# Kernel tuning notes

Measured on AMD Instinct MI355X. Metric: run time of the kernel, lower is better.

The kernel has to match this reference:

```python
import jax, jax.numpy as jnp
import numpy as np

N_EMBD = 1024
HEAD_SIZE = 64

def setup_inputs() -> dict:
    key = jax.random.key(0)
    kx, kk, kq, kv = jax.random.split(key, 4)
    B, T = 8, 2048
    x = jax.random.normal(kx, (B, T, N_EMBD), dtype=jnp.float32)
    s = 1.0 / np.sqrt(N_EMBD)  # torch Linear default init scale (kaiming-uniform-ish)
    Wk = jax.random.uniform(kk, (N_EMBD, HEAD_SIZE), jnp.float32, -s, s)
    Wq = jax.random.uniform(kq, (N_EMBD, HEAD_SIZE), jnp.float32, -s, s)
    Wv = jax.random.uniform(kv, (N_EMBD, HEAD_SIZE), jnp.float32, -s, s)
    return {"x": x, "Wk": Wk, "Wq": Wq, "Wv": Wv}

def reference(x, Wk, Wq, Wv):
    # x: (B,T,C); projections to (B,T,H)
    k = jnp.einsum('btc,ch->bth', x, Wk)
    q = jnp.einsum('btc,ch->bth', x, Wq)
    v = jnp.einsum('btc,ch->bth', x, Wv)
    T = x.shape[1]
    scale = k.shape[-1] ** -0.5
    wei = jnp.einsum('bth,bsh->bts', q, k) * scale  # (B,T,T)
    causal = jnp.tril(jnp.ones((T, T), dtype=bool))
    wei = jnp.where(causal, wei, -jnp.inf)
    wei = jax.nn.softmax(wei, axis=-1)
    out = jnp.einsum('bts,bsh->bth', wei, v)  # (B,T,H)
    return out
```

## Files before the change

kernel.cpp:

```cpp
#include <hip/hip_runtime.h>
#include <math.h>

namespace {
constexpr int BATCH = 8;
constexpr int TSEQ  = 2048;
constexpr int CDIM  = 1024;
constexpr int HDIM  = 64;
constexpr int MROWS = BATCH * TSEQ;
constexpr int NTILE = 128;
constexpr int NSLC  = 4;
constexpr float QSCALE = 0.125f * 1.4426950408889634f;
}

typedef __attribute__((ext_vector_type(4))) float  f32x4;
typedef __attribute__((ext_vector_type(8))) short  s16x8;
typedef __attribute__((ext_vector_type(4))) unsigned short u16x4;

__device__ __forceinline__ unsigned short f2bf(float f) {
    union { float f; unsigned u; } c{f};
    unsigned r = c.u + 0x7FFFu + ((c.u >> 16) & 1u);
    return (unsigned short)(r >> 16);
}

__global__ __launch_bounds__(256)
void wswz_kernel(const float* __restrict__ Wk, const float* __restrict__ Wq,
                 const float* __restrict__ Wv, unsigned short* __restrict__ swz)
{
    const int idx  = blockIdx.x * 256 + threadIdx.x;
    const int j    = idx & 7;
    const int lane = (idx >> 3) & 63;
    const int rest = idx >> 9;
    const int tn   = rest % 12;
    const int ksg  = rest / 12;
    const int kk   = ksg * 32 + (lane >> 4) * 8 + j;
    const int n    = tn * 16 + (lane & 15);
    float val;
    if (n < 64)       val = Wq[kk * HDIM + n] * QSCALE;
    else if (n < 128) val = Wk[kk * HDIM + (n - 64)];
    else              val = Wv[kk * HDIM + (n - 128)];
    swz[idx] = f2bf(val);
}

__global__ __launch_bounds__(512, 4)
void proj_kernel(const float* __restrict__ x, const unsigned short* __restrict__ swz,
                 unsigned short* __restrict__ q, unsigned short* __restrict__ k,
                 unsigned short* __restrict__ vt)
{
    __shared__ unsigned short xl[32][1032];

    const int tid  = threadIdx.x;
    const int lane = tid & 63, wave = tid >> 6;
    const int quad = lane >> 4, l15 = lane & 15;
    const int mh   = wave >> 2;
    const int cq   = wave & 3;
    const int m0   = blockIdx.x * 32;

    {
        const float* xb = x + (size_t)m0 * CDIM;
        float4 t[16];
        #pragma unroll
        for (int i = 0; i < 16; ++i)
            t[i] = *(const float4*)(xb + i * 2048 + tid * 4);
        #pragma unroll
        for (int i = 0; i < 16; ++i) {
            const int o = i * 2048 + tid * 4;
            u16x4 p;
            p[0] = f2bf(t[i].x); p[1] = f2bf(t[i].y);
            p[2] = f2bf(t[i].z); p[3] = f2bf(t[i].w);
            *(u16x4*)&xl[o >> 10][o & 1023] = p;
        }
    }
    __syncthreads();

    f32x4 acc[3] = {};
    const unsigned short* bp = swz + ((size_t)(cq * 3) * 64 + lane) * 8;
    s16x8 b0 = *(const s16x8*)(bp);
    s16x8 b1 = *(const s16x8*)(bp + 512);
    s16x8 b2 = *(const s16x8*)(bp + 1024);
    bp += 6144;

    #pragma unroll
    for (int ks = 0; ks < 32; ++ks) {
        s16x8 nb0, nb1, nb2;
        if (ks < 31) {
            nb0 = *(const s16x8*)(bp);
            nb1 = *(const s16x8*)(bp + 512);
            nb2 = *(const s16x8*)(bp + 1024);
            bp += 6144;
        }
        const s16x8 af = *(const s16x8*)&xl[mh * 16 + l15][ks * 32 + quad * 8];
        acc[0] = __builtin_amdgcn_mfma_f32_16x16x32_bf16(af, b0, acc[0], 0, 0, 0);
        acc[1] = __builtin_amdgcn_mfma_f32_16x16x32_bf16(af, b1, acc[1], 0, 0, 0);
        acc[2] = __builtin_amdgcn_mfma_f32_16x16x32_bf16(af, b2, acc[2], 0, 0, 0);
        if (ks < 31) { b0 = nb0; b1 = nb1; b2 = nb2; }
    }

    const int rowg = m0 + mh * 16 + quad * 4;
    #pragma unroll
    for (int t = 0; t < 3; ++t) {
        const int n = cq * 48 + t * 16 + l15;
        if (n < 64) {
            #pragma unroll
            for (int r = 0; r < 4; ++r)
                q[(size_t)(rowg + r) * HDIM + n] = f2bf(acc[t][r]);
        } else if (n < 128) {
            #pragma unroll
            for (int r = 0; r < 4; ++r)
                k[(size_t)(rowg + r) * HDIM + (n - 64)] = f2bf(acc[t][r]);
        } else {
            const int h  = n - 128;
            const int bb = rowg >> 11, tl = rowg & 2047;
            u16x4 pv;
            #pragma unroll
            for (int r = 0; r < 4; ++r) pv[r] = f2bf(acc[t][r]);
            *(u16x4*)(vt + ((size_t)bb * HDIM + h) * TSEQ + tl) = pv;
        }
    }
}

__global__ __launch_bounds__(256, 2)
void attn_part(const unsigned short* __restrict__ q, const unsigned short* __restrict__ k,
               const unsigned short* __restrict__ vt, float* __restrict__ Opart,
               float* __restrict__ lpart)
{
    __shared__ unsigned short Kb[2][4096];
    __shared__ unsigned short Vb[2][4096];
    __shared__ unsigned short Pl[4][16][72];

    const int tid  = threadIdx.x;
    const int lane = tid & 63, wave = tid >> 6;
    const int quad = lane >> 4, l15 = lane & 15;
    const int b    = blockIdx.y;
    const int p    = blockIdx.x >> 2;
    const int s    = blockIdx.x & 3;

    const unsigned short* qb  = q  + (size_t)b * TSEQ * HDIM;
    const unsigned short* kb  = k  + (size_t)b * TSEQ * HDIM;
    const unsigned short* vtb = vt + (size_t)b * HDIM * TSEQ;

    const int rs = tid >> 3, cgs = tid & 7;
    const int d0 = (((cgs >> 2) * 4 + (rs >> 4)) * 64 + (cgs & 3) * 16 + (rs & 15)) * 8;
    const int rs2 = rs + 32;
    const int d1 = (((cgs >> 2) * 4 + (rs2 >> 4)) * 64 + (cgs & 3) * 16 + (rs2 & 15)) * 8;

    for (int tsel = 0; tsel < 2; ++tsel) {
        const int t   = (tsel == 0) ? p : 31 - p;
        const int m0w = t * 64 + wave * 16;
        const int nt  = t + 1;

        s16x8 aq0 = *(const s16x8*)(qb + (size_t)(m0w + l15) * HDIM + quad * 8);
        s16x8 aq1 = *(const s16x8*)(qb + (size_t)(m0w + l15) * HDIM + 32 + quad * 8);

        f32x4 O[4] = {};
        float l_lane[4] = {0.f, 0.f, 0.f, 0.f};

        if (s < nt) {
            {
                const int n0 = s * 64;
                const s16x8 ka = *(const s16x8*)(kb + (size_t)(n0 + rs) * HDIM + cgs * 8);
                const s16x8 kc = *(const s16x8*)(kb + (size_t)(n0 + rs2) * HDIM + cgs * 8);
                const s16x8 va = *(const s16x8*)(vtb + (size_t)rs * TSEQ + n0 + cgs * 8);
                const s16x8 vc = *(const s16x8*)(vtb + (size_t)rs2 * TSEQ + n0 + cgs * 8);
                *(s16x8*)&Kb[0][d0] = ka; *(s16x8*)&Kb[0][d1] = kc;
                *(s16x8*)&Vb[0][d0] = va; *(s16x8*)&Vb[0][d1] = vc;
            }
            __syncthreads();

            int cur = 0;
            for (int c = s; c < nt; c += 4) {
                const int cn = c + 4;
                const bool pref = cn < nt;
                s16x8 ka, kc, va, vc;
                if (pref) {
                    const int n0n = cn * 64;
                    ka = *(const s16x8*)(kb + (size_t)(n0n + rs) * HDIM + cgs * 8);
                    kc = *(const s16x8*)(kb + (size_t)(n0n + rs2) * HDIM + cgs * 8);
                    va = *(const s16x8*)(vtb + (size_t)rs * TSEQ + n0n + cgs * 8);
                    vc = *(const s16x8*)(vtb + (size_t)rs2 * TSEQ + n0n + cgs * 8);
                }

                const unsigned short* Kc = Kb[cur];
                const unsigned short* Vc = Vb[cur];
                f32x4 S[4] = {};
                #pragma unroll
                for (int st = 0; st < 4; ++st) {
                    const s16x8 k0 = *(const s16x8*)&Kc[(st * 64 + lane) * 8];
                    const s16x8 k1 = *(const s16x8*)&Kc[((4 + st) * 64 + lane) * 8];
                    S[st] = __builtin_amdgcn_mfma_f32_16x16x32_bf16(aq0, k0, S[st], 0, 0, 0);
                    S[st] = __builtin_amdgcn_mfma_f32_16x16x32_bf16(aq1, k1, S[st], 0, 0, 0);
                }

                const int n0 = c * 64;
                if (c == t) {
                    const int rowbase = m0w + quad * 4;
                    #pragma unroll
                    for (int st = 0; st < 4; ++st) {
                        const int col = n0 + st * 16 + l15;
                        #pragma unroll
                        for (int r = 0; r < 4; ++r) {
                            const float pv = (col > rowbase + r) ? 0.f : exp2f(S[st][r]);
                            S[st][r] = pv;
                            l_lane[r] += pv;
                        }
                    }
                } else {
                    #pragma unroll
                    for (int st = 0; st < 4; ++st)
                        #pragma unroll
                        for (int r = 0; r < 4; ++r) {
                            const float pv = exp2f(S[st][r]);
                            S[st][r] = pv;
                            l_lane[r] += pv;
                        }
                }

                #pragma unroll
                for (int st = 0; st < 4; ++st)
                    #pragma unroll
                    for (int r = 0; r < 4; ++r)
                        Pl[wave][quad * 4 + r][st * 16 + l15] = f2bf(S[st][r]);
                const s16x8 pa0 = *(const s16x8*)&Pl[wave][l15][quad * 8];
                const s16x8 pa1 = *(const s16x8*)&Pl[wave][l15][32 + quad * 8];

                #pragma unroll
                for (int hst = 0; hst < 4; ++hst) {
                    const s16x8 v0 = *(const s16x8*)&Vc[(hst * 64 + lane) * 8];
                    const s16x8 v1 = *(const s16x8*)&Vc[((4 + hst) * 64 + lane) * 8];
                    O[hst] = __builtin_amdgcn_mfma_f32_16x16x32_bf16(pa0, v0, O[hst], 0, 0, 0);
                    O[hst] = __builtin_amdgcn_mfma_f32_16x16x32_bf16(pa1, v1, O[hst], 0, 0, 0);
                }

                if (pref) {
                    *(s16x8*)&Kb[1 - cur][d0] = ka; *(s16x8*)&Kb[1 - cur][d1] = kc;
                    *(s16x8*)&Vb[1 - cur][d0] = va; *(s16x8*)&Vb[1 - cur][d1] = vc;
                }
                __syncthreads();
                cur ^= 1;
            }
        }

        #pragma unroll
        for (int off = 1; off < 16; off <<= 1)
            #pragma unroll
            for (int r = 0; r < 4; ++r)
                l_lane[r] += __shfl_xor(l_lane[r], off);

        const int ti16 = t * 4 + wave;
        const size_t pi = ((size_t)b * NTILE + ti16) * NSLC + s;
        #pragma unroll
        for (int hst = 0; hst < 4; ++hst)
            #pragma unroll
            for (int r = 0; r < 4; ++r)
                Opart[(pi * 16 + quad * 4 + r) * HDIM + hst * 16 + l15] = O[hst][r];
        if (l15 == 0) {
            #pragma unroll
            for (int r = 0; r < 4; ++r)
                lpart[pi * 16 + quad * 4 + r] = l_lane[r];
        }
    }
}

__global__ __launch_bounds__(256)
void attn_combine(const float* __restrict__ Opart, const float* __restrict__ lpart,
                  float* __restrict__ out)
{
    const int g   = blockIdx.x * 256 + threadIdx.x;
    const int row = g >> 4;
    const int c4  = (g & 15) << 2;
    const int b   = row >> 11, t = row & 2047;
    const int ti  = t >> 4,  r = t & 15;
    const size_t p0 = ((size_t)b * NTILE + ti) * NSLC;

    float4 acc = {0.f, 0.f, 0.f, 0.f};
    float lv = 0.f;
    #pragma unroll
    for (int s = 0; s < NSLC; ++s) {
        const float4 t4 = *(const float4*)(Opart + ((p0 + s) * 16 + r) * HDIM + c4);
        acc.x += t4.x; acc.y += t4.y; acc.z += t4.z; acc.w += t4.w;
        lv += lpart[(p0 + s) * 16 + r];
    }
    const float inv = 1.f / lv;
    float4 o = {acc.x * inv, acc.y * inv, acc.z * inv, acc.w * inv};
    *(float4*)(out + (size_t)row * HDIM + c4) = o;
}

extern "C" void kernel_launch(void* const* d_in, const int* in_sizes, int n_in,
                              void* d_out, int out_size, void* d_ws, size_t ws_size,
                              hipStream_t stream) {
    const float* x  = (const float*)d_in[0];
    const float* Wk = (const float*)d_in[1];
    const float* Wq = (const float*)d_in[2];
    const float* Wv = (const float*)d_in[3];
    float* out = (float*)d_out;

    unsigned short* swz = (unsigned short*)d_ws;
    unsigned short* qw  = swz + 196608;
    unsigned short* kw  = qw + (size_t)MROWS * HDIM;
    unsigned short* vtw = kw + (size_t)MROWS * HDIM;
    float* Opart = (float*)(vtw + (size_t)MROWS * HDIM);
    float* lpart = Opart + (size_t)BATCH * NTILE * NSLC * 16 * HDIM;

    wswz_kernel<<<dim3(768), 256, 0, stream>>>(Wk, Wq, Wv, swz);
    proj_kernel<<<dim3(MROWS / 32), 512, 0, stream>>>(x, swz, qw, kw, vtw);
    attn_part<<<dim3(16 * NSLC, BATCH), 256, 0, stream>>>(qw, kw, vtw, Opart, lpart);
    attn_combine<<<dim3(MROWS * 16 / 256), 256, 0, stream>>>(Opart, lpart, out);
}
```

Baseline: 136.8 us.

## Double KV split count, single-buffer attention LDS, halve projection block size

The attention partial kernel now splits each query tile's key range across 8 slices instead of 4. This doubles the grid, and the KV tiles drop from double-buffered to single-buffered shared memory with extra barriers around the refill, so more blocks can be resident per CU. The projection kernel now uses 256-thread blocks covering 16 rows instead of 512-thread blocks covering 32 rows. The aim is higher occupancy and more parallelism for the short causal rows. The cost is more partial outputs for the combine kernel to merge and less overlap of loads with compute inside each block.

```diff
diff --git a/kernel.cpp b/kernel.cpp
--- a/kernel.cpp
+++ b/kernel.cpp
@@ -8,7 +8,7 @@
 constexpr int HDIM  = 64;
 constexpr int MROWS = BATCH * TSEQ;
 constexpr int NTILE = 128;
-constexpr int NSLC  = 4;
+constexpr int NSLC  = 8;
 constexpr float QSCALE = 0.125f * 1.4426950408889634f;
 }
 
@@ -41,29 +41,28 @@
     swz[idx] = f2bf(val);
 }
 
-__global__ __launch_bounds__(512, 4)
+__global__ __launch_bounds__(256, 4)
 void proj_kernel(const float* __restrict__ x, const unsigned short* __restrict__ swz,
                  unsigned short* __restrict__ q, unsigned short* __restrict__ k,
                  unsigned short* __restrict__ vt)
 {
-    __shared__ unsigned short xl[32][1032];
+    __shared__ unsigned short xl[16][1032];
 
     const int tid  = threadIdx.x;
     const int lane = tid & 63, wave = tid >> 6;
     const int quad = lane >> 4, l15 = lane & 15;
-    const int mh   = wave >> 2;
-    const int cq   = wave & 3;
-    const int m0   = blockIdx.x * 32;
+    const int cq   = wave;
+    const int m0   = blockIdx.x * 16;
 
     {
         const float* xb = x + (size_t)m0 * CDIM;
         float4 t[16];
         #pragma unroll
         for (int i = 0; i < 16; ++i)
-            t[i] = *(const float4*)(xb + i * 2048 + tid * 4);
+            t[i] = *(const float4*)(xb + i * 1024 + tid * 4);
         #pragma unroll
         for (int i = 0; i < 16; ++i) {
-            const int o = i * 2048 + tid * 4;
+            const int o = i * 1024 + tid * 4;
             u16x4 p;
             p[0] = f2bf(t[i].x); p[1] = f2bf(t[i].y);
             p[2] = f2bf(t[i].z); p[3] = f2bf(t[i].w);
@@ -88,14 +87,14 @@
             nb2 = *(const s16x8*)(bp + 1024);
             bp += 6144;
         }
-        const s16x8 af = *(const s16x8*)&xl[mh * 16 + l15][ks * 32 + quad * 8];
+        const s16x8 af = *(const s16x8*)&xl[l15][ks * 32 + quad * 8];
         acc[0] = __builtin_amdgcn_mfma_f32_16x16x32_bf16(af, b0, acc[0], 0, 0, 0);
         acc[1] = __builtin_amdgcn_mfma_f32_16x16x32_bf16(af, b1, acc[1], 0, 0, 0);
         acc[2] = __builtin_amdgcn_mfma_f32_16x16x32_bf16(af, b2, acc[2], 0, 0, 0);
         if (ks < 31) { b0 = nb0; b1 = nb1; b2 = nb2; }
     }
 
-    const int rowg = m0 + mh * 16 + quad * 4;
+    const int rowg = m0 + quad * 4;
     #pragma unroll
     for (int t = 0; t < 3; ++t) {
         const int n = cq * 48 + t * 16 + l15;
@@ -118,21 +117,21 @@
     }
 }
 
-__global__ __launch_bounds__(256, 2)
+__global__ __launch_bounds__(256, 4)
 void attn_part(const unsigned short* __restrict__ q, const unsigned short* __restrict__ k,
                const unsigned short* __restrict__ vt, float* __restrict__ Opart,
                float* __restrict__ lpart)
 {
-    __shared__ unsigned short Kb[2][4096];
-    __shared__ unsigned short Vb[2][4096];
+    __shared__ unsigned short Kb[4096];
+    __shared__ unsigned short Vb[4096];
     __shared__ unsigned short Pl[4][16][72];
 
     const int tid  = threadIdx.x;
     const int lane = tid & 63, wave = tid >> 6;
     const int quad = lane >> 4, l15 = lane & 15;
     const int b    = blockIdx.y;
-    const int p    = blockIdx.x >> 2;
-    const int s    = blockIdx.x & 3;
+    const int p    = blockIdx.x >> 3;
+    const int s    = blockIdx.x & 7;
 
     const unsigned short* qb  = q  + (size_t)b * TSEQ * HDIM;
     const unsigned short* kb  = k  + (size_t)b * TSEQ * HDIM;
@@ -148,8 +147,8 @@
         const int m0w = t * 64 + wave * 16;
         const int nt  = t + 1;
 
-        s16x8 aq0 = *(const s16x8*)(qb + (size_t)(m0w + l15) * HDIM + quad * 8);
-        s16x8 aq1 = *(const s16x8*)(qb + (size_t)(m0w + l15) * HDIM + 32 + quad * 8);
+        const s16x8 aq0 = *(const s16x8*)(qb + (size_t)(m0w + l15) * HDIM + quad * 8);
+        const s16x8 aq1 = *(const s16x8*)(qb + (size_t)(m0w + l15) * HDIM + 32 + quad * 8);
 
         f32x4 O[4] = {};
         float l_lane[4] = {0.f, 0.f, 0.f, 0.f};
@@ -161,14 +160,13 @@
                 const s16x8 kc = *(const s16x8*)(kb + (size_t)(n0 + rs2) * HDIM + cgs * 8);
                 const s16x8 va = *(const s16x8*)(vtb + (size_t)rs * TSEQ + n0 + cgs * 8);
                 const s16x8 vc = *(const s16x8*)(vtb + (size_t)rs2 * TSEQ + n0 + cgs * 8);
-                *(s16x8*)&Kb[0][d0] = ka; *(s16x8*)&Kb[0][d1] = kc;
-                *(s16x8*)&Vb[0][d0] = va; *(s16x8*)&Vb[0][d1] = vc;
+                *(s16x8*)&Kb[d0] = ka; *(s16x8*)&Kb[d1] = kc;
+                *(s16x8*)&Vb[d0] = va; *(s16x8*)&Vb[d1] = vc;
             }
             __syncthreads();
 
-            int cur = 0;
-            for (int c = s; c < nt; c += 4) {
-                const int cn = c + 4;
+            for (int c = s; c < nt; c += 8) {
+                const int cn = c + 8;
                 const bool pref = cn < nt;
                 s16x8 ka, kc, va, vc;
                 if (pref) {
@@ -179,13 +177,11 @@
                     vc = *(const s16x8*)(vtb + (size_t)rs2 * TSEQ + n0n + cgs * 8);
                 }
 
-                const unsigned short* Kc = Kb[cur];
-                const unsigned short* Vc = Vb[cur];
                 f32x4 S[4] = {};
                 #pragma unroll
                 for (int st = 0; st < 4; ++st) {
-                    const s16x8 k0 = *(const s16x8*)&Kc[(st * 64 + lane) * 8];
-                    const s16x8 k1 = *(const s16x8*)&Kc[((4 + st) * 64 + lane) * 8];
+                    const s16x8 k0 = *(const s16x8*)&Kb[(st * 64 + lane) * 8];
+                    const s16x8 k1 = *(const s16x8*)&Kb[((4 + st) * 64 + lane) * 8];
                     S[st] = __builtin_amdgcn_mfma_f32_16x16x32_bf16(aq0, k0, S[st], 0, 0, 0);
                     S[st] = __builtin_amdgcn_mfma_f32_16x16x32_bf16(aq1, k1, S[st], 0, 0, 0);
                 }
@@ -224,19 +220,20 @@
 
                 #pragma unroll
                 for (int hst = 0; hst < 4; ++hst) {
-                    const s16x8 v0 = *(const s16x8*)&Vc[(hst * 64 + lane) * 8];
-                    const s16x8 v1 = *(const s16x8*)&Vc[((4 + hst) * 64 + lane) * 8];
+                    const s16x8 v0 = *(const s16x8*)&Vb[(hst * 64 + lane) * 8];
+                    const s16x8 v1 = *(const s16x8*)&Vb[((4 + hst) * 64 + lane) * 8];
                     O[hst] = __builtin_amdgcn_mfma_f32_16x16x32_bf16(pa0, v0, O[hst], 0, 0, 0);
                     O[hst] = __builtin_amdgcn_mfma_f32_16x16x32_bf16(pa1, v1, O[hst], 0, 0, 0);
                 }
 
                 if (pref) {
-                    *(s16x8*)&Kb[1 - cur][d0] = ka; *(s16x8*)&Kb[1 - cur][d1] = kc;
-                    *(s16x8*)&Vb[1 - cur][d0] = va; *(s16x8*)&Vb[1 - cur][d1] = vc;
-                }
-                __syncthreads();
-                cur ^= 1;
+                    __syncthreads();
+                    *(s16x8*)&Kb[d0] = ka; *(s16x8*)&Kb[d1] = kc;
+                    *(s16x8*)&Vb[d0] = va; *(s16x8*)&Vb[d1] = vc;
+                    __syncthreads();
+                }
             }
+            __syncthreads();
         }
 
         #pragma unroll
@@ -301,7 +298,7 @@
     float* lpart = Opart + (size_t)BATCH * NTILE * NSLC * 16 * HDIM;
 
     wswz_kernel<<<dim3(768), 256, 0, stream>>>(Wk, Wq, Wv, swz);
-    proj_kernel<<<dim3(MROWS / 32), 512, 0, stream>>>(x, swz, qw, kw, vtw);
+    proj_kernel<<<dim3(MROWS / 16), 256, 0, stream>>>(x, swz, qw, kw, vtw);
     attn_part<<<dim3(16 * NSLC, BATCH), 256, 0, stream>>>(qw, kw, vtw, Opart, lpart);
     attn_combine<<<dim3(MROWS * 16 / 256), 256, 0, stream>>>(Opart, lpart, out);
 }
```

After: 140.1 us. 1.02x slower.
